# Performance work log

Measured on AMD Instinct MI355X. Metric: run time of the kernel, lower is better.

## Reference

```python
import jax, jax.numpy as jnp
import numpy as np

B, T, H, DI, DO = 512, 512, 100, 101, 2
DT_OVER_TAU = 0.1  # dt=1, tau=10


def retanh(x):
    return jnp.maximum(jnp.tanh(x), 0.0)


def setup_inputs() -> dict:
    key = jax.random.key(0)
    k0, k1, k2, k3 = jax.random.split(key, 4)
    inp = jax.random.normal(k0, (B, T, DI), jnp.float32)
    noise = jax.random.normal(k1, (B, T, H), jnp.float32) * 0.1
    W_x_ah = (jax.random.normal(k2, (H, DI), jnp.float32) / np.sqrt(DI)).astype(jnp.float32)
    b_ah = jnp.zeros((H,), jnp.float32)
    # orthogonalized recurrent weights (svd with unit singular values), as in __init__
    A = np.random.default_rng(0).standard_normal((H, H))
    u, _, vT = np.linalg.svd(A)
    W_h_ah = jnp.asarray(u @ vT, jnp.float32)
    # original inits W_h_y to zeros; use small random so output is nontrivial
    W_h_y = jax.random.normal(k3, (DO, H), jnp.float32) * 0.1
    ah0 = jnp.zeros((H,), jnp.float32)
    return {"input": inp, "noise": noise, "W_x_ah": W_x_ah, "b_ah": b_ah,
            "W_h_ah": W_h_ah, "W_h_y": W_h_y, "ah0": ah0}


def reference(input, noise, W_x_ah, b_ah, W_h_ah, W_h_y, ah0):
    # precompute input projection as one batched GEMM: [B,T,H]
    xp = jnp.einsum('bti,hi->bth', input, W_x_ah) + b_ah
    ah_init = jnp.broadcast_to(ah0, (input.shape[0], ah0.shape[0]))
    h_init = retanh(ah_init)

    def step(carry, xs):
        ah, h = carry
        xp_t, nz_t = xs
        ah = ah + DT_OVER_TAU * (-ah + h @ W_h_ah.T + xp_t)
        h = retanh(ah) + nz_t
        return (ah, h), h

    _, hstore = jax.lax.scan(step, (ah_init, h_init),
                             (xp.transpose(1, 0, 2), noise.transpose(1, 0, 2)))
    hstore = hstore.transpose(1, 0, 2)  # [B,T,H]
    output = hstore @ W_h_y.T  # [B,T,DO]
    return output, hstore
```

## Files before the change

### kernel.cpp

```cpp
#include <hip/hip_runtime.h>
#include <hip/hip_bf16.h>

#define BB 512
#define TT 512
#define HH 100
#define DI 101
#define DOUT 2
#define BT (BB * TT)

typedef float f4 __attribute__((ext_vector_type(4)));

__global__ void k_prep(const float* __restrict__ Wx, float* __restrict__ WxP) {
  const int t = threadIdx.x;
  for (int idx = t; idx < HH * 104; idx += 256) {
    const int r = idx / 104;
    const int c = idx - r * 104;
    WxP[idx] = (c < DI) ? Wx[r * DI + c] : 0.f;
  }
}

__global__ __launch_bounds__(128, 2) void k_inproj(
    const float* __restrict__ in, const float* __restrict__ WxP,
    const float* __restrict__ bias, float* __restrict__ xp) {
  const int t = threadIdx.x;
  const int p = t >> 1;
  const int kh = t & 1;
  const int c0 = p;
  const int c1 = p + 64;
  const bool c1ok = (c1 < HH);

  __shared__ __align__(16) float Atile[64 * 104];

  f4 wx0[13], wx1[13];
  {
    const f4* w0p = (const f4*)(WxP + (size_t)c0 * 104 + kh * 52);
    const f4* w1p = (const f4*)(WxP + (size_t)(c1ok ? c1 : 0) * 104 + kh * 52);
#pragma unroll
    for (int j = 0; j < 13; ++j) {
      wx0[j] = w0p[j];
      wx1[j] = w1p[j];
    }
  }
  const float bs0 = bias[c0];
  const float bs1 = c1ok ? bias[c1] : 0.f;

  const int row0 = blockIdx.x * 64;

  {
    const f4* src = (const f4*)(in + (size_t)row0 * DI);
#pragma unroll
    for (int j = 0; j < 13; ++j) {
      const int Q = j * 128 + t;
      if (Q < 1616) {
        f4 v = src[Q];
        const int m = 4 * Q;
#pragma unroll
        for (int kcomp = 0; kcomp < 4; ++kcomp) {
          const int mi = m + kcomp;
          const int r = mi / 101;
          const int c = mi - r * 101;
          Atile[r * 104 + c] = v[kcomp];
        }
      }
    }
    if (t < 64) {
      Atile[t * 104 + 101] = 0.f;
      Atile[t * 104 + 102] = 0.f;
      Atile[t * 104 + 103] = 0.f;
    }
  }
  __syncthreads();

#pragma unroll 2
  for (int r = 0; r < 64; ++r) {
    const f4* a4 = (const f4*)(Atile + r * 104 + kh * 52);
    f4 s0 = {0.f, 0.f, 0.f, 0.f};
    f4 s1 = {0.f, 0.f, 0.f, 0.f};
#pragma unroll
    for (int j = 0; j < 13; ++j) {
      f4 av = a4[j];
      s0 = __builtin_elementwise_fma(av, wx0[j], s0);
      s1 = __builtin_elementwise_fma(av, wx1[j], s1);
    }
    float p0 = (s0.x + s0.y) + (s0.z + s0.w);
    float p1 = (s1.x + s1.y) + (s1.z + s1.w);
    p0 += __shfl_xor(p0, 1, 64);
    p1 += __shfl_xor(p1, 1, 64);
    if (kh == 0) {
      float* xr = xp + (size_t)(row0 + r) * HH;
      xr[c0] = p0 + bs0;
      if (c1ok) xr[c1] = p1 + bs1;
    }
  }
}

__global__ __launch_bounds__(64, 1) void k_scan(
    const float* __restrict__ noise, const float* __restrict__ Wh,
    const float* __restrict__ ah0, const float* __restrict__ Wy,
    float* __restrict__ out, float* hstore ) {
  const int b = blockIdx.x;
  const int l = threadIdx.x;
  const bool act = (l < 50);
  const int s0 = act ? 2 * l : 0;

  __shared__ __align__(16) float h_lds[HH];

  f4 w0[25], w1[25];
  {
    const f4* r0 = (const f4*)(Wh + (size_t)s0 * HH);
    const f4* r1 = (const f4*)(Wh + (size_t)(s0 + 1) * HH);
#pragma unroll
    for (int j = 0; j < 25; ++j) {
      w0[j] = r0[j];
      w1[j] = r1[j];
    }
#pragma unroll
    for (int j = 0; j < 25; ++j) {
      asm volatile("" : "+v"(w0[j]), "+v"(w1[j]));
    }
  }
  float wy00 = 0.f, wy01 = 0.f, wy10 = 0.f, wy11 = 0.f;
  if (act) {
    float2 wa = *(const float2*)(Wy + s0);
    float2 wb = *(const float2*)(Wy + HH + s0);
    wy00 = wa.x; wy01 = wa.y; wy10 = wb.x; wy11 = wb.y;
  }

  float ahx = 0.f, ahy = 0.f;
  if (act) {
    float2 a = *(const float2*)(ah0 + s0);
    ahx = a.x; ahy = a.y;
  }
  {
    float e0 = __expf(-2.f * ahx);
    float e1 = __expf(-2.f * ahy);
    float h0 = (ahx > 0.f) ? (1.f - e0) * __builtin_amdgcn_rcpf(1.f + e0) : 0.f;
    float h1 = (ahy > 0.f) ? (1.f - e1) * __builtin_amdgcn_rcpf(1.f + e1) : 0.f;
    if (act) *(float2*)&h_lds[s0] = make_float2(h0, h1);
  }

  const float* xp_base = hstore;
  const size_t bbase = (size_t)b * TT * HH;
  float2* out2 = (float2*)out;

  float2 xpA = make_float2(0.f, 0.f), nzA = xpA;
  float2 xpB = xpA, nzB = xpA, xpC = xpA, nzC = xpA, xpD = xpA, nzD = xpA;
  if (act) {
    xpA = *(const float2*)(xp_base + bbase + (size_t)0 * HH + s0);
    nzA = *(const float2*)(noise + bbase + (size_t)0 * HH + s0);
    xpB = *(const float2*)(xp_base + bbase + (size_t)1 * HH + s0);
    nzB = *(const float2*)(noise + bbase + (size_t)1 * HH + s0);
    xpC = *(const float2*)(xp_base + bbase + (size_t)2 * HH + s0);
    nzC = *(const float2*)(noise + bbase + (size_t)2 * HH + s0);
    xpD = *(const float2*)(xp_base + bbase + (size_t)3 * HH + s0);
    nzD = *(const float2*)(noise + bbase + (size_t)3 * HH + s0);
  }

#define STEP(XP, NZ, tc)                                                      \
  {                                                                           \
    const int tpf = (tc) + 4;                                                 \
    float2 nxp = make_float2(0.f, 0.f), nnz = nxp;                            \
    if (act && tpf < TT) {                                                    \
      nxp = *(const float2*)(xp_base + bbase + (size_t)tpf * HH + s0);        \
      nnz = *(const float2*)(noise + bbase + (size_t)tpf * HH + s0);          \
    }                                                                         \
    const f4* h4 = (const f4*)h_lds;                                          \
    f4 a0e = {0.f, 0.f, 0.f, 0.f}, a0o = a0e;                                 \
    f4 a1e = a0e, a1o = a0e;                                                  \
    _Pragma("unroll") for (int j = 0; j < 24; j += 2) {                       \
      f4 hvE = h4[j];                     \
      f4 hvO = h4[j + 1];                                                     \
      a0e = __builtin_elementwise_fma(w0[j], hvE, a0e);                       \
      a1e = __builtin_elementwise_fma(w1[j], hvE, a1e);                       \
      a0o = __builtin_elementwise_fma(w0[j + 1], hvO, a0o);                   \
      a1o = __builtin_elementwise_fma(w1[j + 1], hvO, a1o);                   \
    }                                                                         \
    {                                                                         \
      f4 hvL = h4[24];                                                        \
      a0e = __builtin_elementwise_fma(w0[24], hvL, a0e);                      \
      a1e = __builtin_elementwise_fma(w1[24], hvL, a1e);                      \
    }                                                                         \
    f4 acc0 = a0e + a0o;                                                      \
    f4 acc1 = a1e + a1o;                                                      \
    float d0 = (acc0.x + acc0.y) + (acc0.z + acc0.w);                         \
    float d1 = (acc1.x + acc1.y) + (acc1.z + acc1.w);                         \
    ahx = fmaf(0.1f, (d0 + XP.x) - ahx, ahx);                                 \
    ahy = fmaf(0.1f, (d1 + XP.y) - ahy, ahy);                                 \
    float e0 = __expf(-2.f * ahx);                                            \
    float e1 = __expf(-2.f * ahy);                                            \
    float h0 = (ahx > 0.f) ? (1.f - e0) * __builtin_amdgcn_rcpf(1.f + e0)     \
                           : 0.f;                                             \
    float h1 = (ahy > 0.f) ? (1.f - e1) * __builtin_amdgcn_rcpf(1.f + e1)     \
                           : 0.f;                                             \
    h0 += NZ.x;                                                               \
    h1 += NZ.y;                                                               \
             \
    if (act) {                                                                \
      *(float2*)&h_lds[s0] = make_float2(h0, h1);                             \
      *(float2*)(hstore + bbase + (size_t)(tc)*HH + s0) =                     \
          make_float2(h0, h1);                                                \
    }                                                                         \
               \
    float po0 = act ? fmaf(h0, wy00, h1 * wy01) : 0.f;                        \
    float po1 = act ? fmaf(h0, wy10, h1 * wy11) : 0.f;                        \
    po0 += __shfl_xor(po0, 1, 64);                                            \
    po1 += __shfl_xor(po1, 1, 64);                                            \
    po0 += __shfl_xor(po0, 2, 64);                                            \
    po1 += __shfl_xor(po1, 2, 64);                                            \
    po0 += __shfl_xor(po0, 4, 64);                                            \
    po1 += __shfl_xor(po1, 4, 64);                                            \
    po0 += __shfl_xor(po0, 8, 64);                                            \
    po1 += __shfl_xor(po1, 8, 64);                                            \
    po0 += __shfl_xor(po0, 16, 64);                                           \
    po1 += __shfl_xor(po1, 16, 64);                                           \
    po0 += __shfl_xor(po0, 32, 64);                                           \
    po1 += __shfl_xor(po1, 32, 64);                                           \
    if (l == 0) out2[(size_t)b * TT + (tc)] = make_float2(po0, po1);          \
    XP = nxp;                                                                 \
    NZ = nnz;                                                                 \
  }

#pragma unroll 1
  for (int tc = 0; tc < TT; tc += 4) {
    STEP(xpA, nzA, tc);
    STEP(xpB, nzB, tc + 1);
    STEP(xpC, nzC, tc + 2);
    STEP(xpD, nzD, tc + 3);
  }
#undef STEP
}

extern "C" void kernel_launch(void* const* d_in, const int* in_sizes, int n_in,
                              void* d_out, int out_size, void* d_ws,
                              size_t ws_size, hipStream_t stream) {
  const float* input = (const float*)d_in[0];
  const float* noise = (const float*)d_in[1];
  const float* W_x = (const float*)d_in[2];
  const float* b_ah = (const float*)d_in[3];
  const float* W_h = (const float*)d_in[4];
  const float* W_y = (const float*)d_in[5];
  const float* ah0 = (const float*)d_in[6];

  float* out = (float*)d_out;
  float* hstore = out + (size_t)BB * TT * DOUT;
  float* WxP = (float*)d_ws;

  k_prep<<<1, 256, 0, stream>>>(W_x, WxP);

  k_inproj<<<BT / 64, 128, 0, stream>>>(input, WxP, b_ah, hstore);

  k_scan<<<BB, 64, 0, stream>>>(noise, W_h, ah0, W_y, out, hstore);
}
```

Measured before the change: 757.9 us.

## Move output projection out of the recurrent scan into a separate kernel

```diff
diff --git a/kernel.cpp b/kernel.cpp
--- a/kernel.cpp
+++ b/kernel.cpp
@@ -40,6 +40,10 @@
       wx0[j] = w0p[j];
       wx1[j] = w1p[j];
     }
+#pragma unroll
+    for (int j = 0; j < 13; ++j) {
+      asm volatile("" : "+v"(wx0[j]), "+v"(wx1[j]));
+    }
   }
   const float bs0 = bias[c0];
   const float bs1 = c1ok ? bias[c1] : 0.f;
@@ -84,8 +88,10 @@
     }
     float p0 = (s0.x + s0.y) + (s0.z + s0.w);
     float p1 = (s1.x + s1.y) + (s1.z + s1.w);
-    p0 += __shfl_xor(p0, 1, 64);
-    p1 += __shfl_xor(p1, 1, 64);
+    p0 += __int_as_float(__builtin_amdgcn_mov_dpp(
+        __float_as_int(p0), 0xB1, 0xF, 0xF, true));
+    p1 += __int_as_float(__builtin_amdgcn_mov_dpp(
+        __float_as_int(p1), 0xB1, 0xF, 0xF, true));
     if (kh == 0) {
       float* xr = xp + (size_t)(row0 + r) * HH;
       xr[c0] = p0 + bs0;
@@ -96,8 +102,7 @@
 
 __global__ __launch_bounds__(64, 1) void k_scan(
     const float* __restrict__ noise, const float* __restrict__ Wh,
-    const float* __restrict__ ah0, const float* __restrict__ Wy,
-    float* __restrict__ out, float* hstore ) {
+    const float* __restrict__ ah0, float* hstore ) {
   const int b = blockIdx.x;
   const int l = threadIdx.x;
   const bool act = (l < 50);
@@ -118,12 +123,6 @@
     for (int j = 0; j < 25; ++j) {
       asm volatile("" : "+v"(w0[j]), "+v"(w1[j]));
     }
-  }
-  float wy00 = 0.f, wy01 = 0.f, wy10 = 0.f, wy11 = 0.f;
-  if (act) {
-    float2 wa = *(const float2*)(Wy + s0);
-    float2 wb = *(const float2*)(Wy + HH + s0);
-    wy00 = wa.x; wy01 = wa.y; wy10 = wb.x; wy11 = wb.y;
   }
 
   float ahx = 0.f, ahy = 0.f;
@@ -141,7 +140,6 @@
 
   const float* xp_base = hstore;
   const size_t bbase = (size_t)b * TT * HH;
-  float2* out2 = (float2*)out;
 
   float2 xpA = make_float2(0.f, 0.f), nzA = xpA;
   float2 xpB = xpA, nzB = xpA, xpC = xpA, nzC = xpA, xpD = xpA, nzD = xpA;
@@ -200,22 +198,6 @@
       *(float2*)(hstore + bbase + (size_t)(tc)*HH + s0) =                     \
           make_float2(h0, h1);                                                \
     }                                                                         \
-               \
-    float po0 = act ? fmaf(h0, wy00, h1 * wy01) : 0.f;                        \
-    float po1 = act ? fmaf(h0, wy10, h1 * wy11) : 0.f;                        \
-    po0 += __shfl_xor(po0, 1, 64);                                            \
-    po1 += __shfl_xor(po1, 1, 64);                                            \
-    po0 += __shfl_xor(po0, 2, 64);                                            \
-    po1 += __shfl_xor(po1, 2, 64);                                            \
-    po0 += __shfl_xor(po0, 4, 64);                                            \
-    po1 += __shfl_xor(po1, 4, 64);                                            \
-    po0 += __shfl_xor(po0, 8, 64);                                            \
-    po1 += __shfl_xor(po1, 8, 64);                                            \
-    po0 += __shfl_xor(po0, 16, 64);                                           \
-    po1 += __shfl_xor(po1, 16, 64);                                           \
-    po0 += __shfl_xor(po0, 32, 64);                                           \
-    po1 += __shfl_xor(po1, 32, 64);                                           \
-    if (l == 0) out2[(size_t)b * TT + (tc)] = make_float2(po0, po1);          \
     XP = nxp;                                                                 \
     NZ = nnz;                                                                 \
   }
@@ -228,6 +210,43 @@
     STEP(xpD, nzD, tc + 3);
   }
 #undef STEP
+}
+
+__global__ __launch_bounds__(256, 2) void k_outproj(
+    const float* __restrict__ hstore, const float* __restrict__ Wy,
+    float* __restrict__ out) {
+  __shared__ __align__(16) float wy_l[2][HH];
+  const int t = threadIdx.x;
+  if (t < 2 * HH) {
+    int r = t / HH;
+    int c = t - r * HH;
+    wy_l[r][c] = Wy[t];
+  }
+  __syncthreads();
+
+  const int row = blockIdx.x * 256 + t;
+  const float4* h4 = (const float4*)(hstore + (size_t)row * HH);
+  const float4* w0 = (const float4*)wy_l[0];
+  const float4* w1 = (const float4*)wy_l[1];
+  float4 a0 = make_float4(0.f, 0.f, 0.f, 0.f);
+  float4 a1 = make_float4(0.f, 0.f, 0.f, 0.f);
+#pragma unroll
+  for (int j = 0; j < 25; ++j) {
+    float4 hv = h4[j];
+    float4 x0 = w0[j];
+    float4 x1 = w1[j];
+    a0.x = fmaf(hv.x, x0.x, a0.x);
+    a0.y = fmaf(hv.y, x0.y, a0.y);
+    a0.z = fmaf(hv.z, x0.z, a0.z);
+    a0.w = fmaf(hv.w, x0.w, a0.w);
+    a1.x = fmaf(hv.x, x1.x, a1.x);
+    a1.y = fmaf(hv.y, x1.y, a1.y);
+    a1.z = fmaf(hv.z, x1.z, a1.z);
+    a1.w = fmaf(hv.w, x1.w, a1.w);
+  }
+  float d0 = (a0.x + a0.y) + (a0.z + a0.w);
+  float d1 = (a1.x + a1.y) + (a1.z + a1.w);
+  ((float2*)out)[row] = make_float2(d0, d1);
 }
 
 extern "C" void kernel_launch(void* const* d_in, const int* in_sizes, int n_in,
@@ -249,5 +268,7 @@
 
   k_inproj<<<BT / 64, 128, 0, stream>>>(input, WxP, b_ah, hstore);
 
-  k_scan<<<BB, 64, 0, stream>>>(noise, W_h, ah0, W_y, out, hstore);
-}
+  k_scan<<<BB, 64, 0, stream>>>(noise, W_h, ah0, hstore);
+
+  k_outproj<<<BT / 256, 256, 0, stream>>>(hstore, W_y, out);
+}
```

After: 672.6 us. 1.13x faster.
